# Performance work log

Measured on AMD Instinct MI355X. Metric: run time of the kernel, lower is better.

Reference implementation:

```python
import jax, jax.numpy as jnp
import numpy as np

N_NODES = 100000


def _gcn_conv(x, W, b, src, dst, dinv):
    # PyG GCNConv: h = X @ W; out[i] = sum_{j->i} norm_ji * h[j] (incl. self-loop); + b
    h = x @ W                                   # [N, F_out]
    norm = dinv[src] * dinv[dst]                # [E]
    agg = jax.ops.segment_sum(norm[:, None] * h[src], dst, num_segments=N_NODES)
    agg = agg + (dinv * dinv)[:, None] * h      # self-loop contribution
    return agg + b


def setup_inputs() -> dict:
    key = jax.random.key(0)
    ks = jax.random.split(key, 12)
    N, E, F = N_NODES, 3200000, 128

    def glorot(k, fan_in, fan_out):
        s = float(np.sqrt(6.0 / (fan_in + fan_out)))
        return jax.random.uniform(k, (fan_in, fan_out), jnp.float32, -s, s)

    x = jax.random.normal(ks[0], (N, F), jnp.float32)
    edge_index = jax.random.randint(ks[1], (2, E), 0, N, jnp.int64)
    return {
        "x": x,
        "edge_index": edge_index,
        "W1": glorot(ks[2], F, 64),  "b1": jnp.zeros((64,), jnp.float32),
        "W2": glorot(ks[3], 64, 32), "b2": jnp.zeros((32,), jnp.float32),
        "W3": glorot(ks[4], 32, 16), "b3": jnp.zeros((16,), jnp.float32),
        "Ws02": glorot(ks[5], F, 32),  "bs02": jnp.zeros((32,), jnp.float32),
        "Ws03": glorot(ks[6], F, 16),  "bs03": jnp.zeros((16,), jnp.float32),
        "Ws13": glorot(ks[7], 64, 16), "bs13": jnp.zeros((16,), jnp.float32),
    }


def reference(x, edge_index, W1, b1, W2, b2, W3, b3, Ws02, bs02, Ws03, bs03, Ws13, bs13):
    src, dst = edge_index[0], edge_index[1]
    # symmetric GCN normalization with self-loops: deg[i] = 1 + in-degree(i)
    deg = jax.ops.segment_sum(jnp.ones_like(dst, dtype=x.dtype), dst, num_segments=N_NODES) + 1.0
    dinv = jax.lax.rsqrt(deg)

    # eval-mode: dropout is identity
    x1 = jax.nn.relu(_gcn_conv(x, W1, b1, src, dst, dinv))            # [N, 64]
    x2 = jax.nn.relu(_gcn_conv(x1, W2, b2, src, dst, dinv)) + (x @ Ws02 + bs02)   # [N, 32]
    x3 = (jax.nn.relu(_gcn_conv(x2, W3, b3, src, dst, dinv))
          + (x @ Ws03 + bs03) + (x1 @ Ws13 + bs13))                   # [N, 16]
    return x3
```

## Files before the change

### kernel.cpp

```cpp
#include <hip/hip_runtime.h>

#define NN 100000
#define NB 256
#define NPB 391
#define MSCH 4096
#define BCAP 14592

__device__ inline unsigned short f2bf(float f) {
    unsigned u = __float_as_uint(f);
    return (unsigned short)((u + 0x7FFFu + ((u >> 16) & 1u)) >> 16);
}
__device__ inline unsigned packbf(float a, float b) {
    return (unsigned)f2bf(a) | ((unsigned)f2bf(b) << 16);
}
__device__ inline float bflo(unsigned u) { return __uint_as_float(u << 16); }
__device__ inline float bfhi(unsigned u) { return __uint_as_float(u & 0xFFFF0000u); }
__device__ inline float4 bf4(uint2 u) {
    return make_float4(bflo(u.x), bfhi(u.x), bflo(u.y), bfhi(u.y));
}

__device__ inline void fp8acc(unsigned u, float4& a) {
    auto lo = __builtin_amdgcn_cvt_pk_f32_fp8((int)u, false);
    auto hi = __builtin_amdgcn_cvt_pk_f32_fp8((int)u, true);
    a.x += lo[0]; a.y += lo[1]; a.z += hi[0]; a.w += hi[1];
}
__device__ inline unsigned char f2fp8(float v) {
    return (unsigned char)(__builtin_amdgcn_cvt_pk_fp8_f32(v, 0.f, 0, false) & 0xFF);
}
__device__ inline unsigned short f2fp8x2(float a, float b) {
    return (unsigned short)(__builtin_amdgcn_cvt_pk_fp8_f32(a, b, 0, false) & 0xFFFF);
}

typedef __attribute__((ext_vector_type(8))) short bf16x8;
typedef __attribute__((ext_vector_type(4))) float f32x4;


__global__ __launch_bounds__(256) void multisplit_kernel(const int* __restrict__ src, const int* __restrict__ dst,
                                                         int E, int* __restrict__ cursors,
                                                         unsigned int* __restrict__ packed) {
    __shared__ unsigned stage_p[MSCH];
    __shared__ unsigned char stage_b[MSCH];
    __shared__ int cnt[NB];
    __shared__ int base[NB];
    int t = threadIdx.x;
    for (long c0 = (long)blockIdx.x * MSCH; c0 < E; c0 += (long)gridDim.x * MSCH) {
        if (t < NB) cnt[t] = 0;
        __syncthreads();
        int nE = (int)min((long)MSCH, E - c0);
        for (int k = t; k < nE; k += 256) {
            int d = dst[c0 + k];
            int s = src[c0 + k];
            int b = d / NPB;
            int ld = d - b * NPB;
            atomicAdd(&cnt[b], 1);
            stage_p[k] = ((unsigned)s << 9) | (unsigned)ld;
            stage_b[k] = (unsigned char)b;
        }
        __syncthreads();
        if (t < NB) base[t] = cnt[t] ? atomicAdd(&cursors[t], cnt[t]) : 0;
        __syncthreads();
        for (int k = t; k < nE; k += 256) {
            int b = stage_b[k];
            int pos = atomicAdd(&base[b], 1);
            packed[pos] = stage_p[k];
        }
        __syncthreads();
    }
}

__global__ __launch_bounds__(NB) void bstart_kernel(const int* __restrict__ cursors, int* __restrict__ bstart, int E) {
    __shared__ int sh[NB];
    int t = threadIdx.x;
    int v = cursors[t] - t * BCAP;
    sh[t] = v;
    __syncthreads();
    for (int off = 1; off < NB; off <<= 1) {
        int u = (t >= off) ? sh[t - off] : 0;
        __syncthreads();
        sh[t] += u;
        __syncthreads();
    }
    bstart[t] = sh[t] - v;
    if (t == NB - 1) bstart[NB] = E;
}

__global__ __launch_bounds__(512) void bucket_fill_kernel(const unsigned int* __restrict__ packed,
                                                          const int* __restrict__ bstart, int N, int E,
                                                          int* __restrict__ rowptr, int* __restrict__ col,
                                                          float* __restrict__ dinv) {
    int b = blockIdx.x, t = threadIdx.x;
    int e0d = bstart[b], cnt = bstart[b + 1] - e0d;
    long e0s = (long)b * BCAP;
    __shared__ int hist[512];
    __shared__ int sh[512];
    __shared__ int cur[512];
    hist[t] = 0;
    __syncthreads();
    for (int e = t; e < cnt; e += 512)
        atomicAdd(&hist[packed[e0s + e] & 511u], 1);
    __syncthreads();
    int v = hist[t];
    sh[t] = v;
    __syncthreads();
    for (int off = 1; off < 512; off <<= 1) {
        int u = (t >= off) ? sh[t - off] : 0;
        __syncthreads();
        sh[t] += u;
        __syncthreads();
    }
    int ex = sh[t] - v;
    int node = b * NPB + t;
    if (t < NPB && node < N) {
        rowptr[node] = e0d + ex;
        dinv[node] = rsqrtf(1.0f + (float)v);
    }
    cur[t] = e0d + ex;
    __syncthreads();
    for (int e = t; e < cnt; e += 512) {
        unsigned int p = packed[e0s + e];
        int pos = atomicAdd(&cur[p & 511u], 1);
        col[pos] = (int)(p >> 9);
    }
    if (b == 0 && t == 0) rowptr[N] = E;
}


__global__ __launch_bounds__(256) void wpack_kernel(const float* __restrict__ W1, const float* __restrict__ Ws02,
                                                    const float* __restrict__ Ws03, unsigned short* __restrict__ Wpk,
                                                    int* __restrict__ cursors) {
    if (blockIdx.x == 0 && threadIdx.x < NB) cursors[threadIdx.x] = threadIdx.x * BCAP;
    int i = blockIdx.x * 256 + threadIdx.x;
    if (i >= 112 * 128) return;
    int c = i >> 7, k = i & 127;
    float v;
    if (c < 64)      v = W1[k * 64 + c];
    else if (c < 96) v = Ws02[k * 32 + (c - 64)];
    else             v = Ws03[k * 16 + (c - 96)];
    Wpk[i] = f2bf(v);
}


__global__ __launch_bounds__(256) void mfma3_kernel(const float* __restrict__ X,
        const unsigned short* __restrict__ Wpk, const float* __restrict__ scale,
        const float* __restrict__ bb, const float* __restrict__ bc,
        unsigned char* __restrict__ oa, unsigned short* __restrict__ ob,
        unsigned short* __restrict__ oc, int N) {
    int t = threadIdx.x;
    int wv = t >> 6, l = t & 63;
    int r0 = blockIdx.x * 128 + wv * 32;
    int col = l & 15, g = l >> 4;
    int rowA0 = r0 + col, rowA1 = r0 + 16 + col;
    bool ok0 = rowA0 < N, ok1 = rowA1 < N;
    const float* xr0 = X + (size_t)rowA0 * 128;
    const float* xr1 = X + (size_t)rowA1 * 128;

    f32x4 acc[2][7];
    #pragma unroll
    for (int ti = 0; ti < 2; ++ti)
        #pragma unroll
        for (int i = 0; i < 7; ++i) acc[ti][i] = (f32x4){0.f, 0.f, 0.f, 0.f};

    #pragma unroll
    for (int s = 0; s < 4; ++s) {
        int k0 = s * 32 + g * 8;
        float4 lo0 = ok0 ? *(const float4*)(xr0 + k0)     : make_float4(0.f, 0.f, 0.f, 0.f);
        float4 hi0 = ok0 ? *(const float4*)(xr0 + k0 + 4) : make_float4(0.f, 0.f, 0.f, 0.f);
        float4 lo1 = ok1 ? *(const float4*)(xr1 + k0)     : make_float4(0.f, 0.f, 0.f, 0.f);
        float4 hi1 = ok1 ? *(const float4*)(xr1 + k0 + 4) : make_float4(0.f, 0.f, 0.f, 0.f);
        union { bf16x8 v; unsigned u[4]; } A0, A1;
        A0.u[0] = packbf(lo0.x, lo0.y); A0.u[1] = packbf(lo0.z, lo0.w);
        A0.u[2] = packbf(hi0.x, hi0.y); A0.u[3] = packbf(hi0.z, hi0.w);
        A1.u[0] = packbf(lo1.x, lo1.y); A1.u[1] = packbf(lo1.z, lo1.w);
        A1.u[2] = packbf(hi1.x, hi1.y); A1.u[3] = packbf(hi1.z, hi1.w);
        #pragma unroll
        for (int ct = 0; ct < 7; ++ct) {
            bf16x8 B = *(const bf16x8*)(Wpk + ((size_t)(ct * 16 + col) * 128 + k0));
            acc[0][ct] = __builtin_amdgcn_mfma_f32_16x16x32_bf16(A0.v, B, acc[0][ct], 0, 0, 0);
            acc[1][ct] = __builtin_amdgcn_mfma_f32_16x16x32_bf16(A1.v, B, acc[1][ct], 0, 0, 0);
        }
    }

    #pragma unroll
    for (int ti = 0; ti < 2; ++ti) {
        #pragma unroll
        for (int v = 0; v < 4; ++v) {
            int row = r0 + ti * 16 + g * 4 + v;
            if (row < N) {
                float sc = scale[row];
                #pragma unroll
                for (int ct = 0; ct < 4; ++ct)
                    oa[(size_t)row * 64 + ct * 16 + col] = f2fp8(acc[ti][ct][v] * sc);
                #pragma unroll
                for (int ct = 4; ct < 6; ++ct) {
                    int c2 = (ct - 4) * 16 + col;
                    ob[(size_t)row * 32 + c2] = f2bf(acc[ti][ct][v] + bb[c2]);
                }
                oc[(size_t)row * 16 + col] = f2bf(acc[ti][6][v] + bc[col]);
            }
        }
    }
}


template <int K, int C1, int C2>
__global__ __launch_bounds__(256) void gemm2b_kernel(const unsigned short* __restrict__ X,
        const float* __restrict__ Wa, const float* __restrict__ scale,
        const float* __restrict__ Wb, const float* __restrict__ bb,
        unsigned char* __restrict__ oa, unsigned short* __restrict__ ob, int N) {
    constexpr int M1 = C1 / 16, M2 = C2 / 16;
    constexpr int XS = K + 6;
    __shared__ float XL[64 * XS];
    __shared__ float WLa[K * C1];
    __shared__ float WLb[K * C2];
    int t = threadIdx.x;
    int r0 = blockIdx.x * 64;

    for (int i = t; i < K * C1 / 4; i += 256) ((float4*)WLa)[i] = ((const float4*)Wa)[i];
    for (int i = t; i < K * C2 / 4; i += 256) ((float4*)WLb)[i] = ((const float4*)Wb)[i];
    for (int i = t; i < 64 * (K / 4); i += 256) {
        int row = i / (K / 4), g = i % (K / 4);
        uint2 u = make_uint2(0u, 0u);
        if (r0 + row < N) u = ((const uint2*)(X + (size_t)(r0 + row) * K))[g];
        float* p = &XL[row * XS + g * 4];
        *(float2*)p = make_float2(bflo(u.x), bfhi(u.x));
        *(float2*)(p + 2) = make_float2(bflo(u.y), bfhi(u.y));
    }
    __syncthreads();

    int ty = t >> 4, tx = t & 15;
    float acc1[4][M1] = {}, acc2[4][M2] = {};
    const float* xb = &XL[(ty * 4) * XS];
    const float* wba = &WLa[tx * M1];
    const float* wbb = &WLb[tx * M2];
    for (int k = 0; k < K; ++k) {
        float x0 = xb[k], x1 = xb[XS + k], x2 = xb[2 * XS + k], x3 = xb[3 * XS + k];
        float wa[M1], wb2[M2];
        #pragma unroll
        for (int j = 0; j < M1; ++j) wa[j] = wba[k * C1 + j];
        #pragma unroll
        for (int j = 0; j < M2; ++j) wb2[j] = wbb[k * C2 + j];
        #pragma unroll
        for (int j = 0; j < M1; ++j) {
            acc1[0][j] = fmaf(x0, wa[j], acc1[0][j]);
            acc1[1][j] = fmaf(x1, wa[j], acc1[1][j]);
            acc1[2][j] = fmaf(x2, wa[j], acc1[2][j]);
            acc1[3][j] = fmaf(x3, wa[j], acc1[3][j]);
        }
        #pragma unroll
        for (int j = 0; j < M2; ++j) {
            acc2[0][j] = fmaf(x0, wb2[j], acc2[0][j]);
            acc2[1][j] = fmaf(x1, wb2[j], acc2[1][j]);
            acc2[2][j] = fmaf(x2, wb2[j], acc2[2][j]);
            acc2[3][j] = fmaf(x3, wb2[j], acc2[3][j]);
        }
    }

    #pragma unroll
    for (int i = 0; i < 4; ++i) {
        int row = r0 + ty * 4 + i;
        if (row < N) {
            float sc = scale[row];
            *(unsigned short*)(oa + (size_t)row * C1 + tx * 2) = f2fp8x2(acc1[i][0] * sc, acc1[i][1] * sc);
            ob[(size_t)row * C2 + tx] = f2bf(acc2[i][0] + bb[tx]);
        }
    }
}


__global__ __launch_bounds__(256) void gemm_l3_kernel(const unsigned short* __restrict__ X,
        const float* __restrict__ W, const float* __restrict__ scale,
        unsigned char* __restrict__ out, int N) {
    constexpr int K = 32, C = 16, XS = K + 6;
    __shared__ float XL[64 * XS];
    __shared__ float WL[K * C];
    int t = threadIdx.x;
    int r0 = blockIdx.x * 64;

    for (int i = t; i < K * C / 4; i += 256) ((float4*)WL)[i] = ((const float4*)W)[i];
    for (int i = t; i < 64 * (K / 4); i += 256) {
        int row = i / (K / 4), g = i % (K / 4);
        uint2 u = make_uint2(0u, 0u);
        if (r0 + row < N) u = ((const uint2*)(X + (size_t)(r0 + row) * K))[g];
        float* p = &XL[row * XS + g * 4];
        *(float2*)p = make_float2(bflo(u.x), bfhi(u.x));
        *(float2*)(p + 2) = make_float2(bflo(u.y), bfhi(u.y));
    }
    __syncthreads();

    int ty = t >> 4, tx = t & 15;
    float acc[4] = {0.f, 0.f, 0.f, 0.f};
    const float* xb = &XL[(ty * 4) * XS];
    for (int k = 0; k < K; ++k) {
        float wv = WL[k * C + tx];
        acc[0] = fmaf(xb[k], wv, acc[0]);
        acc[1] = fmaf(xb[XS + k], wv, acc[1]);
        acc[2] = fmaf(xb[2 * XS + k], wv, acc[2]);
        acc[3] = fmaf(xb[3 * XS + k], wv, acc[3]);
    }
    #pragma unroll
    for (int i = 0; i < 4; ++i) {
        int row = r0 + ty * 4 + i;
        if (row < N) out[(size_t)row * C + tx] = f2fp8(acc[i] * scale[row]);
    }
}


template <int F, int FPL, bool OBF>
__global__ __launch_bounds__(256) void agg_kernel(const unsigned char* __restrict__ hs,
        const int* __restrict__ rowptr, const int* __restrict__ col,
        const float* __restrict__ dinv, const float* __restrict__ bias,
        const unsigned short* __restrict__ skipA, const unsigned short* __restrict__ skipB,
        void* __restrict__ outv, int N) {
    constexpr int VL = F / FPL;
    constexpr int NPW = 64 / VL;
    constexpr int W = 8;
    constexpr int CR = W / VL;
    int t = threadIdx.x;
    int lane = t & 63, wv = t >> 6;
    int sub = lane / VL, fq = lane % VL;
    int i = (blockIdx.x * 4 + wv) * NPW + sub;
    if (i >= N) return;

    float4 aA0 = make_float4(0.f, 0.f, 0.f, 0.f);
    float4 aA1 = make_float4(0.f, 0.f, 0.f, 0.f);
    float4 aB0 = make_float4(0.f, 0.f, 0.f, 0.f);
    float4 aB1 = make_float4(0.f, 0.f, 0.f, 0.f);

    {
        const unsigned char* hrow = hs + (size_t)i * F + fq * FPL;
        if constexpr (FPL == 8) {
            uint2 u = *(const uint2*)hrow;
            fp8acc(u.x, aA0); fp8acc(u.y, aB0);
        } else {
            fp8acc(*(const unsigned*)hrow, aA0);
        }
    }

    int p0 = rowptr[i], p1 = rowptr[i + 1];
    int p = p0;
    for (; p + W <= p1; p += W) {
        int cw[CR];
        #pragma unroll
        for (int j = 0; j < CR; ++j) cw[j] = col[p + fq + j * VL];
        #pragma unroll
        for (int k = 0; k < W; ++k) {
            int s = __shfl(cw[k / VL], k % VL, VL);
            const unsigned char* sp = hs + (size_t)s * F + fq * FPL;
            if constexpr (FPL == 8) {
                uint2 u = *(const uint2*)sp;
                if (k & 1) { fp8acc(u.x, aA1); fp8acc(u.y, aB1); }
                else       { fp8acc(u.x, aA0); fp8acc(u.y, aB0); }
            } else {
                if (k & 1) fp8acc(*(const unsigned*)sp, aA1);
                else       fp8acc(*(const unsigned*)sp, aA0);
            }
        }
    }
    for (; p < p1; p += VL) {
        int c = (p + fq < p1) ? col[p + fq] : 0;
        int m = min(VL, p1 - p);
        for (int k = 0; k < m; ++k) {
            int s = __shfl(c, k, VL);
            const unsigned char* sp = hs + (size_t)s * F + fq * FPL;
            if constexpr (FPL == 8) {
                uint2 u = *(const uint2*)sp;
                fp8acc(u.x, aA1); fp8acc(u.y, aB1);
            } else {
                fp8acc(*(const unsigned*)sp, aA1);
            }
        }
    }

    float di = dinv[i];
    int fb = fq * FPL;
    float o[FPL];
    o[0] = fmaxf(di * (aA0.x + aA1.x) + bias[fb + 0], 0.f);
    o[1] = fmaxf(di * (aA0.y + aA1.y) + bias[fb + 1], 0.f);
    o[2] = fmaxf(di * (aA0.z + aA1.z) + bias[fb + 2], 0.f);
    o[3] = fmaxf(di * (aA0.w + aA1.w) + bias[fb + 3], 0.f);
    if constexpr (FPL == 8) {
        o[4] = fmaxf(di * (aB0.x + aB1.x) + bias[fb + 4], 0.f);
        o[5] = fmaxf(di * (aB0.y + aB1.y) + bias[fb + 5], 0.f);
        o[6] = fmaxf(di * (aB0.z + aB1.z) + bias[fb + 6], 0.f);
        o[7] = fmaxf(di * (aB0.w + aB1.w) + bias[fb + 7], 0.f);
    }
    if (skipA) {
        const unsigned short* sp = skipA + (size_t)i * F + fb;
        if constexpr (FPL == 8) {
            uint4 sa = *(const uint4*)sp;
            float4 s0 = bf4(make_uint2(sa.x, sa.y)), s1 = bf4(make_uint2(sa.z, sa.w));
            o[0] += s0.x; o[1] += s0.y; o[2] += s0.z; o[3] += s0.w;
            o[4] += s1.x; o[5] += s1.y; o[6] += s1.z; o[7] += s1.w;
        } else {
            float4 s0 = bf4(*(const uint2*)sp);
            o[0] += s0.x; o[1] += s0.y; o[2] += s0.z; o[3] += s0.w;
        }
    }
    if (skipB) {
        const unsigned short* sp = skipB + (size_t)i * F + fb;
        if constexpr (FPL == 8) {
            uint4 sa = *(const uint4*)sp;
            float4 s0 = bf4(make_uint2(sa.x, sa.y)), s1 = bf4(make_uint2(sa.z, sa.w));
            o[0] += s0.x; o[1] += s0.y; o[2] += s0.z; o[3] += s0.w;
            o[4] += s1.x; o[5] += s1.y; o[6] += s1.z; o[7] += s1.w;
        } else {
            float4 s0 = bf4(*(const uint2*)sp);
            o[0] += s0.x; o[1] += s0.y; o[2] += s0.z; o[3] += s0.w;
        }
    }

    if constexpr (OBF) {
        unsigned short* op = (unsigned short*)outv + (size_t)i * F + fb;
        if constexpr (FPL == 8) {
            uint4 w4;
            w4.x = packbf(o[0], o[1]); w4.y = packbf(o[2], o[3]);
            w4.z = packbf(o[4], o[5]); w4.w = packbf(o[6], o[7]);
            *(uint4*)op = w4;
        } else {
            uint2 w2;
            w2.x = packbf(o[0], o[1]); w2.y = packbf(o[2], o[3]);
            *(uint2*)op = w2;
        }
    } else {
        *(float4*)((float*)outv + (size_t)i * F + fb) = make_float4(o[0], o[1], o[2], o[3]);
    }
}


extern "C" void kernel_launch(void* const* d_in, const int* in_sizes, int n_in,
                              void* d_out, int out_size, void* d_ws, size_t ws_size,
                              hipStream_t stream) {
    const int N = NN;
    const float* x   = (const float*)d_in[0];
    const int*   ei  = (const int*)d_in[1];
    const int    E   = in_sizes[1] / 2;
    const int*   src = ei;
    const int*   dst = ei + E;
    const float* W1 = (const float*)d_in[2],  *b1  = (const float*)d_in[3];
    const float* W2 = (const float*)d_in[4],  *b2  = (const float*)d_in[5];
    const float* W3 = (const float*)d_in[6],  *b3  = (const float*)d_in[7];
    const float* Ws02 = (const float*)d_in[8],  *bs02 = (const float*)d_in[9];
    const float* Ws03 = (const float*)d_in[10], *bs03 = (const float*)d_in[11];
    const float* Ws13 = (const float*)d_in[12], *bs13 = (const float*)d_in[13];

    char* w = (char*)d_ws;
    size_t off = 0;
    auto alloc = [&](size_t bytes) -> void* {
        void* p = w + off;
        off += (bytes + 255) & ~(size_t)255;
        return p;
    };
    int*   bstart   = (int*)alloc((size_t)(NB + 1) * 4);
    int*   cursors  = (int*)alloc((size_t)NB * 4);
    int*   rowptr   = (int*)alloc(((size_t)N + 1) * 4);
    float* dinv     = (float*)alloc((size_t)N * 4);
    int*   col      = (int*)alloc((size_t)E * 4);
    unsigned short* Wpk = (unsigned short*)alloc((size_t)112 * 128 * 2);
    unsigned char* hs1  = (unsigned char*)alloc((size_t)N * 64 * 2);
    unsigned short* x1  = (unsigned short*)alloc((size_t)N * 64 * 2);
    unsigned short* s02 = (unsigned short*)alloc((size_t)N * 32 * 2);
    unsigned short* s03 = (unsigned short*)alloc((size_t)N * 16 * 2);
    unsigned short* x2  = (unsigned short*)alloc((size_t)N * 32 * 2);
    unsigned int* packed = (unsigned int*)x1;
    unsigned char* hs2 = hs1;
    unsigned short* s13 = (unsigned short*)(hs1 + (size_t)N * 64);
    unsigned char* hs3 = (unsigned char*)s02;

    wpack_kernel<<<(112 * 128 + 255) / 256, 256, 0, stream>>>(W1, Ws02, Ws03, Wpk, cursors);

    multisplit_kernel<<<(E + MSCH - 1) / MSCH, 256, 0, stream>>>(src, dst, E, cursors, packed);
    bstart_kernel<<<1, NB, 0, stream>>>(cursors, bstart, E);
    bucket_fill_kernel<<<NB, 512, 0, stream>>>(packed, bstart, N, E, rowptr, col, dinv);

    int gb = (N + 63) / 64;
    mfma3_kernel<<<(N + 127) / 128, 256, 0, stream>>>(x, Wpk, dinv, bs02, bs03, hs1, s02, s03, N);
    agg_kernel<64, 8, true><<<(N + 31) / 32, 256, 0, stream>>>(hs1, rowptr, col, dinv, b1, nullptr, nullptr, x1, N);
    gemm2b_kernel<64, 32, 16><<<gb, 256, 0, stream>>>(x1, W2, dinv, Ws13, bs13, hs2, s13, N);
    agg_kernel<32, 8, true><<<gb, 256, 0, stream>>>(hs2, rowptr, col, dinv, b2, s02, nullptr, x2, N);
    gemm_l3_kernel<<<gb, 256, 0, stream>>>(x2, W3, dinv, hs3, N);
    agg_kernel<16, 4, false><<<gb, 256, 0, stream>>>(hs3, rowptr, col, dinv, b3, s03, s13, (float*)d_out, N);
}
```

Before: 218.3 us.

## Replace atomic-cursor multisplit with deterministic histogram-scan-scatter bucket partition

Edge bucketing previously used one kernel that staged edges in LDS and claimed space in fixed-capacity buckets through global atomic cursors. It becomes a three-pass radix-style partition: per-chunk bucket histograms, a per-bucket scan across chunks, then a scatter to exact compact offsets. This removes the fixed BCAP slot layout and the contended global atomics, so packed data is contiguous. In exchange dst is read twice and two extra kernel launches plus count and offset arrays are added.

```diff
diff --git a/kernel.cpp b/kernel.cpp
--- a/kernel.cpp
+++ b/kernel.cpp
@@ -4,7 +4,7 @@
 #define NB 256
 #define NPB 391
 #define MSCH 4096
-#define BCAP 14592
+#define NBLK 782
 
 __device__ inline unsigned short f2bf(float f) {
     unsigned u = __float_as_uint(f);
@@ -35,43 +35,56 @@
 typedef __attribute__((ext_vector_type(4))) float f32x4;
 
 
-__global__ __launch_bounds__(256) void multisplit_kernel(const int* __restrict__ src, const int* __restrict__ dst,
-                                                         int E, int* __restrict__ cursors,
-                                                         unsigned int* __restrict__ packed) {
-    __shared__ unsigned stage_p[MSCH];
-    __shared__ unsigned char stage_b[MSCH];
-    __shared__ int cnt[NB];
-    __shared__ int base[NB];
-    int t = threadIdx.x;
-    for (long c0 = (long)blockIdx.x * MSCH; c0 < E; c0 += (long)gridDim.x * MSCH) {
-        if (t < NB) cnt[t] = 0;
+__global__ __launch_bounds__(256) void histA_kernel(const int* __restrict__ dst, int E,
+                                                    int* __restrict__ counts) {
+    __shared__ int h[NB];
+    int t = threadIdx.x, blk = blockIdx.x;
+    h[t] = 0;
+    __syncthreads();
+    long c0 = (long)blk * MSCH;
+    int nE = (int)min((long)MSCH, E - c0);
+    for (int k = t; k < nE; k += 256)
+        atomicAdd(&h[dst[c0 + k] / NPB], 1);
+    __syncthreads();
+    counts[(size_t)blk * NB + t] = h[t];
+}
+
+__global__ __launch_bounds__(256) void bscan2_kernel(const int* __restrict__ counts, int nblk,
+                                                     int* __restrict__ blkoff, int* __restrict__ totals) {
+    int b = blockIdx.x, t = threadIdx.x;
+    const int NP = 4;
+    int c[NP];
+    int s = 0;
+    #pragma unroll
+    for (int q = 0; q < NP; ++q) {
+        int j = t * NP + q;
+        c[q] = (j < nblk) ? counts[(size_t)j * NB + b] : 0;
+        s += c[q];
+    }
+    __shared__ int sh[256];
+    sh[t] = s;
+    __syncthreads();
+    for (int off = 1; off < 256; off <<= 1) {
+        int u = (t >= off) ? sh[t - off] : 0;
         __syncthreads();
-        int nE = (int)min((long)MSCH, E - c0);
-        for (int k = t; k < nE; k += 256) {
-            int d = dst[c0 + k];
-            int s = src[c0 + k];
-            int b = d / NPB;
-            int ld = d - b * NPB;
-            atomicAdd(&cnt[b], 1);
-            stage_p[k] = ((unsigned)s << 9) | (unsigned)ld;
-            stage_b[k] = (unsigned char)b;
-        }
+        sh[t] += u;
         __syncthreads();
-        if (t < NB) base[t] = cnt[t] ? atomicAdd(&cursors[t], cnt[t]) : 0;
-        __syncthreads();
-        for (int k = t; k < nE; k += 256) {
-            int b = stage_b[k];
-            int pos = atomicAdd(&base[b], 1);
-            packed[pos] = stage_p[k];
-        }
-        __syncthreads();
-    }
-}
-
-__global__ __launch_bounds__(NB) void bstart_kernel(const int* __restrict__ cursors, int* __restrict__ bstart, int E) {
+    }
+    int base = sh[t] - s;
+    int run = base;
+    #pragma unroll
+    for (int q = 0; q < NP; ++q) {
+        int j = t * NP + q;
+        if (j < nblk) blkoff[(size_t)j * NB + b] = run;
+        run += c[q];
+    }
+    if (t == 255) totals[b] = sh[255];
+}
+
+__global__ __launch_bounds__(NB) void bstart_kernel(const int* __restrict__ totals, int* __restrict__ bstart, int E) {
     __shared__ int sh[NB];
     int t = threadIdx.x;
-    int v = cursors[t] - t * BCAP;
+    int v = totals[t];
     sh[t] = v;
     __syncthreads();
     for (int off = 1; off < NB; off <<= 1) {
@@ -84,20 +97,39 @@
     if (t == NB - 1) bstart[NB] = E;
 }
 
+__global__ __launch_bounds__(256) void scatter_kernel(const int* __restrict__ src, const int* __restrict__ dst,
+                                                      int E, const int* __restrict__ bstart,
+                                                      const int* __restrict__ blkoff,
+                                                      unsigned int* __restrict__ packed) {
+    __shared__ int base[NB];
+    int t = threadIdx.x, blk = blockIdx.x;
+    base[t] = bstart[t] + blkoff[(size_t)blk * NB + t];
+    __syncthreads();
+    long c0 = (long)blk * MSCH;
+    int nE = (int)min((long)MSCH, E - c0);
+    for (int k = t; k < nE; k += 256) {
+        int d = dst[c0 + k];
+        int s = src[c0 + k];
+        int b = d / NPB;
+        int ld = d - b * NPB;
+        int pos = atomicAdd(&base[b], 1);
+        packed[pos] = ((unsigned)s << 9) | (unsigned)ld;
+    }
+}
+
 __global__ __launch_bounds__(512) void bucket_fill_kernel(const unsigned int* __restrict__ packed,
                                                           const int* __restrict__ bstart, int N, int E,
                                                           int* __restrict__ rowptr, int* __restrict__ col,
                                                           float* __restrict__ dinv) {
     int b = blockIdx.x, t = threadIdx.x;
-    int e0d = bstart[b], cnt = bstart[b + 1] - e0d;
-    long e0s = (long)b * BCAP;
+    int e0 = bstart[b], cnt = bstart[b + 1] - e0;
     __shared__ int hist[512];
     __shared__ int sh[512];
     __shared__ int cur[512];
     hist[t] = 0;
     __syncthreads();
     for (int e = t; e < cnt; e += 512)
-        atomicAdd(&hist[packed[e0s + e] & 511u], 1);
+        atomicAdd(&hist[packed[e0 + e] & 511u], 1);
     __syncthreads();
     int v = hist[t];
     sh[t] = v;
@@ -111,13 +143,13 @@
     int ex = sh[t] - v;
     int node = b * NPB + t;
     if (t < NPB && node < N) {
-        rowptr[node] = e0d + ex;
+        rowptr[node] = e0 + ex;
         dinv[node] = rsqrtf(1.0f + (float)v);
     }
-    cur[t] = e0d + ex;
+    cur[t] = e0 + ex;
     __syncthreads();
     for (int e = t; e < cnt; e += 512) {
-        unsigned int p = packed[e0s + e];
+        unsigned int p = packed[e0 + e];
         int pos = atomicAdd(&cur[p & 511u], 1);
         col[pos] = (int)(p >> 9);
     }
@@ -126,9 +158,7 @@
 
 
 __global__ __launch_bounds__(256) void wpack_kernel(const float* __restrict__ W1, const float* __restrict__ Ws02,
-                                                    const float* __restrict__ Ws03, unsigned short* __restrict__ Wpk,
-                                                    int* __restrict__ cursors) {
-    if (blockIdx.x == 0 && threadIdx.x < NB) cursors[threadIdx.x] = threadIdx.x * BCAP;
+                                                    const float* __restrict__ Ws03, unsigned short* __restrict__ Wpk) {
     int i = blockIdx.x * 256 + threadIdx.x;
     if (i >= 112 * 128) return;
     int c = i >> 7, k = i & 127;
@@ -443,6 +473,8 @@
     const float* Ws03 = (const float*)d_in[10], *bs03 = (const float*)d_in[11];
     const float* Ws13 = (const float*)d_in[12], *bs13 = (const float*)d_in[13];
 
+    const int nblk = (E + MSCH - 1) / MSCH;
+
     char* w = (char*)d_ws;
     size_t off = 0;
     auto alloc = [&](size_t bytes) -> void* {
@@ -451,10 +483,12 @@
         return p;
     };
     int*   bstart   = (int*)alloc((size_t)(NB + 1) * 4);
-    int*   cursors  = (int*)alloc((size_t)NB * 4);
+    int*   totals   = (int*)alloc((size_t)NB * 4);
     int*   rowptr   = (int*)alloc(((size_t)N + 1) * 4);
     float* dinv     = (float*)alloc((size_t)N * 4);
     int*   col      = (int*)alloc((size_t)E * 4);
+    int*   counts   = (int*)alloc((size_t)nblk * NB * 4);
+    int*   blkoff   = (int*)alloc((size_t)nblk * NB * 4);
     unsigned short* Wpk = (unsigned short*)alloc((size_t)112 * 128 * 2);
     unsigned char* hs1  = (unsigned char*)alloc((size_t)N * 64 * 2);
     unsigned short* x1  = (unsigned short*)alloc((size_t)N * 64 * 2);
@@ -466,10 +500,12 @@
     unsigned short* s13 = (unsigned short*)(hs1 + (size_t)N * 64);
     unsigned char* hs3 = (unsigned char*)s02;
 
-    wpack_kernel<<<(112 * 128 + 255) / 256, 256, 0, stream>>>(W1, Ws02, Ws03, Wpk, cursors);
-
-    multisplit_kernel<<<(E + MSCH - 1) / MSCH, 256, 0, stream>>>(src, dst, E, cursors, packed);
-    bstart_kernel<<<1, NB, 0, stream>>>(cursors, bstart, E);
+    wpack_kernel<<<(112 * 128 + 255) / 256, 256, 0, stream>>>(W1, Ws02, Ws03, Wpk);
+
+    histA_kernel<<<nblk, 256, 0, stream>>>(dst, E, counts);
+    bscan2_kernel<<<NB, 256, 0, stream>>>(counts, nblk, blkoff, totals);
+    bstart_kernel<<<1, NB, 0, stream>>>(totals, bstart, E);
+    scatter_kernel<<<nblk, 256, 0, stream>>>(src, dst, E, bstart, blkoff, packed);
     bucket_fill_kernel<<<NB, 512, 0, stream>>>(packed, bstart, N, E, rowptr, col, dinv);
 
     int gb = (N + 63) / 64;
```

Measured after the change: 221.5 us. About the same (+1.4%).
